# Kernel tuning notes

Measured on AMD Instinct MI355X. Metric: run time of the kernel, lower is better.

## Reference

```python
import jax, jax.numpy as jnp
import numpy as np

PATCH = 9  # patch_size (kernel_size=1, stride=1, padding=0, dilation_patch=1)


def setup_inputs() -> dict:
    key = jax.random.key(0)
    k1, k2 = jax.random.split(key)
    B, C, H, W = 4, 256, 128, 128
    return {
        "input1": jax.random.normal(k1, (B, C, H, W), dtype=jnp.float32),
        "input2": jax.random.normal(k2, (B, C, H, W), dtype=jnp.float32),
    }


def _correlation(input1, input2, patch=PATCH):
    # Faithful to torch _correlation_patch_based fast path:
    # corr[b, dy*P+dx, h, w] = sum_c input1[b,c,h,w] * input2_pad[b,c,h+dy,w+dx]
    # where input2 is zero-padded by P//2 (matches F.unfold padding=P//2).
    B, C, H, W = input1.shape
    pad = patch // 2
    i2p = jnp.pad(input2, ((0, 0), (0, 0), (pad, pad), (pad, pad)))
    # displacement offsets in unfold order: ky-major, kx-minor
    offs = jnp.stack(
        jnp.meshgrid(jnp.arange(patch), jnp.arange(patch), indexing="ij"), axis=-1
    ).reshape(-1, 2)  # (P*P, 2)

    def body(carry, off):
        # shifted window of input2, same (B,C,H,W) footprint (no unfold blowup)
        win = jax.lax.dynamic_slice(i2p, (0, 0, off[0], off[1]), (B, C, H, W))
        return carry, jnp.einsum("bchw,bchw->bhw", input1, win)

    _, corr = jax.lax.scan(body, None, offs)  # (P*P, B, H, W)
    return jnp.transpose(corr, (1, 0, 2, 3))  # (B, P*P, H, W)


def reference(input1, input2):
    return _correlation(input1, input2)
```

## Files before the change

### kernel.cpp

```cpp
#include <hip/hip_runtime.h>

#define BB   4
#define CC   256
#define HH   128
#define WW   128
#define PAD  4
#define KOUT 81

#define TH   8
#define SW   16
#define KC   32
#define NCHUNK (CC / KC)
#define AK   40

typedef _Float16 half8 __attribute__((ext_vector_type(8)));
typedef float    f32x4 __attribute__((ext_vector_type(4)));

__global__ __launch_bounds__(512, 3)
void corr_mfma4(const float* __restrict__ i1,
                const float* __restrict__ i2,
                float* __restrict__ out)
{
    __shared__ _Float16 Bld[384 * AK];
    __shared__ _Float16 Ald[128 * AK];

    const int t    = threadIdx.x;
    const int wave = t >> 6;
    const int lane = t & 63;
    const int l15  = lane & 15;
    const int quad = lane >> 4;

    const int b  = blockIdx.z;
    const int h0 = blockIdx.y * TH;
    const int w0 = blockIdx.x * SW;

    const size_t strideC = (size_t)HH * WW;
    const float* i1b = i1 + (size_t)b * CC * strideC;
    const float* i2b = i2 + (size_t)b * CC * strideC;

    const bool isB = (t < 384);
    bool valid;
    int pix;
    _Float16* ldst;
    if (isB) {
        const int sq  = t % 24;
        const int sr  = t / 24;
        const int col = w0 - PAD + sq;
        const int row = h0 - PAD + sr;
        valid = (col >= 0) && (col < WW) && (row >= 0) && (row < HH);
        pix   = valid ? (row * WW + col) : 0;
        ldst  = &Bld[(sr * 24 + sq) * AK];
    } else {
        const int i  = t - 384;
        const int sm = i & 15;
        const int sr = i >> 4;
        valid = true;
        pix   = (h0 + sr) * WW + (w0 + sm);
        ldst  = &Ald[(sr * 16 + sm) * AK];
    }

    f32x4 acc[9][2];
#pragma unroll
    for (int dy = 0; dy < 9; ++dy) {
        acc[dy][0] = (f32x4){0.f, 0.f, 0.f, 0.f};
        acc[dy][1] = (f32x4){0.f, 0.f, 0.f, 0.f};
    }

    float v[KC];

#define LOAD_CHUNK(CH)                                                        \
    do {                                                                      \
        const int c0_ = (CH) * KC;                                            \
        if (isB) {                                                            \
            _Pragma("unroll")                                                 \
            for (int j = 0; j < KC; ++j) {                                    \
                const float* cb = i2b + (size_t)(c0_ + j) * strideC;          \
                float x = cb[pix];                                            \
                v[j] = valid ? x : 0.f;                                       \
            }                                                                 \
        } else {                                                              \
            _Pragma("unroll")                                                 \
            for (int j = 0; j < KC; ++j) {                                    \
                const float* cb = i1b + (size_t)(c0_ + j) * strideC;          \
                v[j] = cb[pix];                                               \
            }                                                                 \
        }                                                                     \
    } while (0)

#define STORE_CHUNK()                                                         \
    do {                                                                      \
        _Pragma("unroll")                                                     \
        for (int u = 0; u < 4; ++u) {                                         \
            half8 hv;                                                         \
            _Pragma("unroll")                                                 \
            for (int k = 0; k < 8; ++k) hv[k] = (_Float16)v[8 * u + k];       \
            *(half8*)&ldst[8 * u] = hv;                                       \
        }                                                                     \
    } while (0)

    LOAD_CHUNK(0);
    STORE_CHUNK();
    __syncthreads();

#pragma unroll 1
    for (int ch = 0; ch < NCHUNK; ++ch) {
        if (ch + 1 < NCHUNK) LOAD_CHUNK(ch + 1);

        {
            const half8 a = *(const half8*)&Ald[(wave * 16 + l15) * AK + quad * 8];
#pragma unroll
            for (int dy = 0; dy < 9; ++dy) {
                const int r = wave + dy;
                const half8 b0 = *(const half8*)&Bld[(r * 24 + l15) * AK + quad * 8];
                acc[dy][0] = __builtin_amdgcn_mfma_f32_16x16x32_f16(a, b0, acc[dy][0], 0, 0, 0);
                const half8 b1 = *(const half8*)&Bld[(r * 24 + 16 + l15) * AK + quad * 8];
                acc[dy][1] = __builtin_amdgcn_mfma_f32_16x16x32_f16(a, b1, acc[dy][1], 0, 0, 0);
            }
        }

        if (ch + 1 < NCHUNK) {
            __syncthreads();
            STORE_CHUNK();
            __syncthreads();
        }
    }

    const int h = h0 + wave;
#pragma unroll
    for (int dy = 0; dy < 9; ++dy) {
#pragma unroll
        for (int tt = 0; tt < 2; ++tt) {
#pragma unroll
            for (int reg = 0; reg < 4; ++reg) {
                const int p  = quad * 4 + reg;
                const int dx = l15 + 16 * tt - p;
                if (dx >= 0 && dx <= 8) {
                    out[(((size_t)b * KOUT + (dy * 9 + dx)) * HH + h) * WW + (w0 + p)] =
                        acc[dy][tt][reg];
                }
            }
        }
    }
#undef LOAD_CHUNK
#undef STORE_CHUNK
}

extern "C" void kernel_launch(void* const* d_in, const int* in_sizes, int n_in,
                              void* d_out, int out_size, void* d_ws, size_t ws_size,
                              hipStream_t stream)
{
    (void)in_sizes; (void)n_in; (void)d_ws; (void)ws_size; (void)out_size;
    const float* i1 = (const float*)d_in[0];
    const float* i2 = (const float*)d_in[1];
    float* out = (float*)d_out;

    dim3 grid(WW / SW, HH / TH, BB);
    dim3 block(512);
    corr_mfma4<<<grid, block, 0, stream>>>(i1, i2, out);
}
```

Before: 190.3 us.

## Pre-convert inputs to channel-chunked fp16 layout in a separate pass

Adds a first kernel that converts both inputs to fp16 and transposes them into a [chunk][pixel][32-channel] layout in the workspace. The correlation kernel then loads each pixel's 32 channels as four contiguous 16-byte vectors, replacing 32 strided scalar fp32 loads and the per-element conversion. Padding pixels are zeroed once in LDS and never reloaded. The cost is an extra kernel launch and an extra full read and half-size write of both inputs through global memory, plus a dependency on the workspace being large enough.

New measurement: 208.9 us. 9.8% more time.

```diff
diff --git a/kernel.cpp b/kernel.cpp
--- a/kernel.cpp
+++ b/kernel.cpp
@@ -6,23 +6,73 @@
 #define WW   128
 #define PAD  4
 #define KOUT 81
+#define KC   32
+#define NCC  (CC / KC)
 
 #define TH   8
 #define SW   16
-#define KC   32
-#define NCHUNK (CC / KC)
 #define AK   40
+#define BPTS 384
+#define APTS 128
+
+#define PLANE      ((size_t)HH * WW)
+#define CHPLANE    (PLANE * KC)
+#define SLOT_ELEMS ((size_t)BB * NCC * CHPLANE)
 
 typedef _Float16 half8 __attribute__((ext_vector_type(8)));
 typedef float    f32x4 __attribute__((ext_vector_type(4)));
 
-__global__ __launch_bounds__(512, 3)
-void corr_mfma4(const float* __restrict__ i1,
+__global__ __launch_bounds__(256)
+void corr_pass1(const float* __restrict__ i1,
                 const float* __restrict__ i2,
+                _Float16* __restrict__ interm)
+{
+    __shared__ float tile[32 * 132];
+
+    const int t   = threadIdx.x;
+    const int h   = blockIdx.x;
+    const int cc  = blockIdx.y;
+    const int zb  = blockIdx.z;
+    const int inp = zb >> 2;
+    const int b   = zb & 3;
+
+    const float* src = (inp ? i2 : i1)
+                     + ((size_t)b * CC + cc * KC) * PLANE + (size_t)h * WW;
+
+    {
+        const int wv = t >> 6;
+        const int ln = t & 63;
+        const int cp = ln >> 5;
+        const int w4 = ln & 31;
+#pragma unroll
+        for (int k = 0; k < 4; ++k) {
+            const int c = wv * 8 + 2 * k + cp;
+            const float4 v = *(const float4*)(src + (size_t)c * PLANE + w4 * 4);
+            *(float4*)&tile[c * 132 + w4 * 4] = v;
+        }
+    }
+    __syncthreads();
+
+    {
+        const int w = t >> 1;
+        const int g = t & 1;
+        _Float16 o[16];
+#pragma unroll
+        for (int j = 0; j < 16; ++j)
+            o[j] = (_Float16)tile[(g * 16 + j) * 132 + w];
+        _Float16* dst = interm + (size_t)inp * SLOT_ELEMS
+                      + ((size_t)(b * NCC + cc) * PLANE + (size_t)h * WW + w) * KC
+                      + g * 16;
+        *(half8*)&dst[0] = *(half8*)&o[0];
+        *(half8*)&dst[8] = *(half8*)&o[8];
+    }
+}
+
+__global__ __launch_bounds__(512)
+void corr_pass2(const _Float16* __restrict__ interm,
                 float* __restrict__ out)
 {
-    __shared__ _Float16 Bld[384 * AK];
-    __shared__ _Float16 Ald[128 * AK];
+    __shared__ _Float16 sh[(BPTS + APTS) * AK];
 
     const int t    = threadIdx.x;
     const int wave = t >> 6;
@@ -34,29 +84,34 @@
     const int h0 = blockIdx.y * TH;
     const int w0 = blockIdx.x * SW;
 
-    const size_t strideC = (size_t)HH * WW;
-    const float* i1b = i1 + (size_t)b * CC * strideC;
-    const float* i2b = i2 + (size_t)b * CC * strideC;
-
-    const bool isB = (t < 384);
+    const bool isB = (t < BPTS);
     bool valid;
-    int pix;
+    size_t pixoff;
     _Float16* ldst;
+    const _Float16* gbase;
     if (isB) {
         const int sq  = t % 24;
         const int sr  = t / 24;
         const int col = w0 - PAD + sq;
         const int row = h0 - PAD + sr;
-        valid = (col >= 0) && (col < WW) && (row >= 0) && (row < HH);
-        pix   = valid ? (row * WW + col) : 0;
-        ldst  = &Bld[(sr * 24 + sq) * AK];
+        valid  = (col >= 0) && (col < WW) && (row >= 0) && (row < HH);
+        pixoff = (size_t)(valid ? row * WW + col : 0) * KC;
+        ldst   = &sh[(sr * 24 + sq) * AK];
+        gbase  = interm + SLOT_ELEMS + (size_t)b * NCC * CHPLANE;
     } else {
-        const int i  = t - 384;
+        const int i  = t - BPTS;
         const int sm = i & 15;
         const int sr = i >> 4;
-        valid = true;
-        pix   = (h0 + sr) * WW + (w0 + sm);
-        ldst  = &Ald[(sr * 16 + sm) * AK];
+        valid  = true;
+        pixoff = (size_t)((h0 + sr) * WW + (w0 + sm)) * KC;
+        ldst   = &sh[(BPTS + sr * 16 + sm) * AK];
+        gbase  = interm + (size_t)b * NCC * CHPLANE;
+    }
+
+    if (!valid) {
+        const int4 z = {0, 0, 0, 0};
+#pragma unroll
+        for (int k = 0; k < 4; ++k) *(int4*)&ldst[k * 8] = z;
     }
 
     f32x4 acc[9][2];
@@ -66,35 +121,20 @@
         acc[dy][1] = (f32x4){0.f, 0.f, 0.f, 0.f};
     }
 
-    float v[KC];
+    int4 vbuf[4];
 
 #define LOAD_CHUNK(CH)                                                        \
     do {                                                                      \
-        const int c0_ = (CH) * KC;                                            \
-        if (isB) {                                                            \
-            _Pragma("unroll")                                                 \
-            for (int j = 0; j < KC; ++j) {                                    \
-                const float* cb = i2b + (size_t)(c0_ + j) * strideC;          \
-                float x = cb[pix];                                            \
-                v[j] = valid ? x : 0.f;                                       \
-            }                                                                 \
-        } else {                                                              \
-            _Pragma("unroll")                                                 \
-            for (int j = 0; j < KC; ++j) {                                    \
-                const float* cb = i1b + (size_t)(c0_ + j) * strideC;          \
-                v[j] = cb[pix];                                               \
-            }                                                                 \
-        }                                                                     \
+        const _Float16* g_ = gbase + (size_t)(CH) * CHPLANE + pixoff;         \
+        _Pragma("unroll")                                                     \
+        for (int k = 0; k < 4; ++k) vbuf[k] = ((const int4*)g_)[k];           \
     } while (0)
 
 #define STORE_CHUNK()                                                         \
     do {                                                                      \
-        _Pragma("unroll")                                                     \
-        for (int u = 0; u < 4; ++u) {                                         \
-            half8 hv;                                                         \
+        if (valid) {                                                          \
             _Pragma("unroll")                                                 \
-            for (int k = 0; k < 8; ++k) hv[k] = (_Float16)v[8 * u + k];       \
-            *(half8*)&ldst[8 * u] = hv;                                       \
+            for (int k = 0; k < 4; ++k) *(int4*)&ldst[k * 8] = vbuf[k];       \
         }                                                                     \
     } while (0)
 
@@ -103,27 +143,29 @@
     __syncthreads();
 
 #pragma unroll 1
-    for (int ch = 0; ch < NCHUNK; ++ch) {
-        if (ch + 1 < NCHUNK) LOAD_CHUNK(ch + 1);
+    for (int ch = 0; ch < NCC; ++ch) {
+        if (ch + 1 < NCC) LOAD_CHUNK(ch + 1);
 
         {
-            const half8 a = *(const half8*)&Ald[(wave * 16 + l15) * AK + quad * 8];
+            const half8 a = *(const half8*)&sh[(BPTS + wave * 16 + l15) * AK + quad * 8];
 #pragma unroll
             for (int dy = 0; dy < 9; ++dy) {
                 const int r = wave + dy;
-                const half8 b0 = *(const half8*)&Bld[(r * 24 + l15) * AK + quad * 8];
+                const half8 b0 = *(const half8*)&sh[(r * 24 + l15) * AK + quad * 8];
                 acc[dy][0] = __builtin_amdgcn_mfma_f32_16x16x32_f16(a, b0, acc[dy][0], 0, 0, 0);
-                const half8 b1 = *(const half8*)&Bld[(r * 24 + 16 + l15) * AK + quad * 8];
+                const half8 b1 = *(const half8*)&sh[(r * 24 + 16 + l15) * AK + quad * 8];
                 acc[dy][1] = __builtin_amdgcn_mfma_f32_16x16x32_f16(a, b1, acc[dy][1], 0, 0, 0);
             }
         }
 
-        if (ch + 1 < NCHUNK) {
+        if (ch + 1 < NCC) {
             __syncthreads();
             STORE_CHUNK();
             __syncthreads();
         }
     }
+#undef LOAD_CHUNK
+#undef STORE_CHUNK
 
     const int h = h0 + wave;
 #pragma unroll
@@ -141,20 +183,21 @@
             }
         }
     }
-#undef LOAD_CHUNK
-#undef STORE_CHUNK
 }
 
 extern "C" void kernel_launch(void* const* d_in, const int* in_sizes, int n_in,
                               void* d_out, int out_size, void* d_ws, size_t ws_size,
                               hipStream_t stream)
 {
-    (void)in_sizes; (void)n_in; (void)d_ws; (void)ws_size; (void)out_size;
+    (void)in_sizes; (void)n_in; (void)ws_size; (void)out_size;
     const float* i1 = (const float*)d_in[0];
     const float* i2 = (const float*)d_in[1];
     float* out = (float*)d_out;
-
-    dim3 grid(WW / SW, HH / TH, BB);
-    dim3 block(512);
-    corr_mfma4<<<grid, block, 0, stream>>>(i1, i2, out);
+    _Float16* interm = (_Float16*)d_ws;
+
+    dim3 g1(HH, NCC, 2 * BB);
+    corr_pass1<<<g1, dim3(256), 0, stream>>>(i1, i2, interm);
+
+    dim3 g2(WW / SW, HH / TH, BB);
+    corr_pass2<<<g2, dim3(512), 0, stream>>>(interm, out);
 }
```
